# Kernel tuning notes

Measured on AMD Instinct MI355X. Metric: run time of the kernel, lower is better.

## Reference

```python
import jax, jax.numpy as jnp
import numpy as np

B, C, CI, H, W = 4, 256, 128, 48, 48
EPS = 1e-5  # BatchNorm2d default eps


def _make_bn(k, n, c):
    kg, kb, km, kv = jax.random.split(k, 4)
    gamma = 1.0 + 0.1 * jax.random.normal(kg, (n, c), jnp.float32)
    beta = 0.1 * jax.random.normal(kb, (n, c), jnp.float32)
    mean = 0.1 * jax.random.normal(km, (n, c), jnp.float32)
    var = 0.5 + jax.random.uniform(kv, (n, c), jnp.float32)
    return jnp.stack([gamma, beta, mean, var], axis=1)  # [n, 4, c]


def setup_inputs() -> dict:
    key = jax.random.key(0)
    ks = jax.random.split(key, 8)
    x1 = jax.random.normal(ks[0], (B, C, H, W), jnp.float32)
    x2 = jax.random.normal(ks[1], (B, C, H, W), jnp.float32)
    bn_pre = _make_bn(ks[2], 4, C)                       # g1, g2, theta, phi pre-BN
    w_pre = 0.05 * jax.random.normal(ks[3], (4, CI, C), jnp.float32)
    b_pre = 0.01 * jax.random.normal(ks[4], (4, CI), jnp.float32)
    w_post = 0.05 * jax.random.normal(ks[5], (2, C, CI), jnp.float32)  # W1, W2 convs
    b_post = 0.01 * jax.random.normal(ks[6], (2, C), jnp.float32)
    bn_post = _make_bn(ks[7], 2, C)                      # W1, W2 post-BN
    return dict(x1=x1, x2=x2, bn_pre=bn_pre, w_pre=w_pre, b_pre=b_pre,
                w_post=w_post, b_post=b_post, bn_post=bn_post)


def _bn(x, p):
    # eval-mode BatchNorm2d: p = [gamma, beta, mean, var], each [C]
    gamma, beta, mean, var = p[0], p[1], p[2], p[3]
    scale = (gamma / jnp.sqrt(var + EPS))[:, None, None]
    return (x - mean[:, None, None]) * scale + beta[:, None, None]


def reference(x1, x2, bn_pre, w_pre, b_pre, w_post, b_post, bn_post):
    Bsz, _, Hh, Ww = x1.shape
    N = Hh * Ww

    def pre(x, i):  # BN -> 1x1 conv -> flatten to [B, CI, N]
        h = _bn(x, bn_pre[i])
        y = jnp.einsum('oc,bchw->bohw', w_pre[i], h) + b_pre[i][None, :, None, None]
        return y.reshape(Bsz, -1, N)

    g11 = pre(x1, 0)   # g1(x1)
    g21 = pre(x2, 1)   # g2(x2)
    th1 = pre(x1, 2)   # theta(x1)
    ph1 = pre(x2, 3)   # phi(x2)

    e_time = jnp.einsum('bcn,bdn->bcd', th1, ph1)    # [B, CI, CI]  (theta @ phi^T)
    e_space = jnp.einsum('bcn,bcm->bnm', th1, ph1)   # [B, N, N]    (theta^T @ phi)

    et1s = jax.nn.softmax(e_time, axis=-1)                          # energy_time_1s
    et2s = jax.nn.softmax(jnp.swapaxes(e_time, 1, 2), axis=-1)      # energy_time_2s
    es2s = jax.nn.softmax(e_space, axis=-2)                         # energy_space_2s
    es1s = jax.nn.softmax(jnp.swapaxes(e_space, 1, 2), axis=-2)     # energy_space_1s

    y1 = jnp.einsum('bcd,bdn,bnm->bcm', et2s, g11, es2s).reshape(Bsz, -1, Hh, Ww)
    y2 = jnp.einsum('bcd,bdn,bnm->bcm', et1s, g21, es1s).reshape(Bsz, -1, Hh, Ww)

    def post(y, i):  # 1x1 conv -> BN
        h = jnp.einsum('oc,bchw->bohw', w_post[i], y) + b_post[i][None, :, None, None]
        return _bn(h, bn_post[i])

    return (x1 + post(y1, 0), x2 + post(y2, 1))
```

## Files before the change

### kernel.cpp

```cpp
#include <hip/hip_runtime.h>
#include <hip/hip_bf16.h>


#define N_PIX 2304
#define NB 4

typedef __attribute__((ext_vector_type(8))) short bf16x8;
typedef __attribute__((ext_vector_type(4))) float f32x4;

__device__ __forceinline__ short f2bf(float f) {
  unsigned u = __float_as_uint(f);
  unsigned r = (u + 0x7fffu + ((u >> 16) & 1u)) >> 16;
  return (short)r;
}
__device__ __forceinline__ float bf2f(short s) {
  return __uint_as_float(((unsigned)(unsigned short)s) << 16);
}
__device__ __forceinline__ int swzf(int row, int kc, int bk64) {
  return bk64 ? (kc ^ ((row ^ (row >> 3)) & 7)) : ((kc ^ (row >> 1)) & 3);
}
__device__ __forceinline__ unsigned pk2(short a, short b) {
  return (unsigned)(unsigned short)a | ((unsigned)(unsigned short)b << 16);
}


struct GArgs {
  const short *a0, *a1, *al0, *al1;
  const short *b0, *b1, *bl0, *bl1;
  long sa, sb, sal, sbl;
  int lda, ldb, lal, lbl;
  int K, ksplit, kchunk;
  int bt0, bt1;
  void *o0, *o1; long so;
  void *p0, *p1; long sp;
  void *q0, *q1; long sq;
  void *u0, *u1; long su;
  const float *aux0, *aux1; long saux;
  const float *res0, *res1; long sres;
};

template <int EPI, int SPLIT, int BK>
__global__ __launch_bounds__(256) void mgemm(GArgs g) {
  constexpr int NCHS = (BK == 64) ? 3 : 2;
  constexpr int ROWSH = (BK == 64) ? 6 : 5;
  constexpr int BK64 = (BK == 64);

  int z = blockIdx.z;
  int pb = z / g.ksplit, ks = z - pb * g.ksplit;
  int sel = pb >> 2, batch = pb & 3;
  const short* A = (sel ? g.a1 : g.a0) + (long)batch * g.sa;
  const short* B = (sel ? g.b1 : g.b0) + (long)batch * g.sb;
  const short* Al = nullptr; const short* Bl = nullptr;
  if (SPLIT) {
    Al = (sel ? g.al1 : g.al0) + (long)batch * g.sal;
    Bl = (sel ? g.bl1 : g.bl0) + (long)batch * g.sbl;
  }
  int bt = sel ? g.bt1 : g.bt0;
  int k0 = ks * g.kchunk, k1 = k0 + g.kchunk;
  int m0 = blockIdx.y << 7, n0 = blockIdx.x << 7;

  __shared__ short As[128 * BK];
  __shared__ short Bs[128 * BK];
  __shared__ short Als[SPLIT ? 128 * BK : 8];
  __shared__ short Bls[SPLIT ? 128 * BK : 8];

  int t = threadIdx.x;
  int lane = t & 63, wid = t >> 6;
  int wm = (wid >> 1) << 6, wn = (wid & 1) << 6;
  int l15 = lane & 15, lg = lane >> 4;

  f32x4 acc[4][4];
  #pragma unroll
  for (int i = 0; i < 4; ++i)
    #pragma unroll
    for (int j = 0; j < 4; ++j) acc[i][j] = (f32x4){0.f, 0.f, 0.f, 0.f};

  for (int kt = k0; kt < k1; kt += BK) {
    __syncthreads();
    #pragma unroll
    for (int i = 0; i < BK / 16; ++i) {
      int ch = t + (i << 8);
      int row = ch >> NCHS, kc = ch & ((BK >> 3) - 1);
      int di = (row << ROWSH) + (swzf(row, kc, BK64) << 3);
      *(bf16x8*)&As[di] = *(const bf16x8*)&A[(long)(m0 + row) * g.lda + kt + (kc << 3)];
      if (SPLIT)
        *(bf16x8*)&Als[di] = *(const bf16x8*)&Al[(long)(m0 + row) * g.lal + kt + (kc << 3)];
    }
    if (BK64 && bt) {
      int nc = t & 15, kq = t >> 4;
      const short* Bp = &B[(long)(kt + (kq << 2)) * g.ldb + n0 + (nc << 3)];
      bf16x8 v0 = *(const bf16x8*)&Bp[0];
      bf16x8 v1 = *(const bf16x8*)&Bp[g.ldb];
      bf16x8 v2 = *(const bf16x8*)&Bp[2 * g.ldb];
      bf16x8 v3 = *(const bf16x8*)&Bp[3 * g.ldb];
      int kc = kq >> 1, wof = (kq & 1) << 2;
      #pragma unroll
      for (int e = 0; e < 8; ++e) {
        int rn = (nc << 3) + e;
        uint2 pkk; pkk.x = pk2(v0[e], v1[e]); pkk.y = pk2(v2[e], v3[e]);
        *(uint2*)&Bs[(rn << 6) + (swzf(rn, kc, 1) << 3) + wof] = pkk;
      }
    } else {
      #pragma unroll
      for (int i = 0; i < BK / 16; ++i) {
        int ch = t + (i << 8);
        int row = ch >> NCHS, kc = ch & ((BK >> 3) - 1);
        int di = (row << ROWSH) + (swzf(row, kc, BK64) << 3);
        *(bf16x8*)&Bs[di] = *(const bf16x8*)&B[(long)(n0 + row) * g.ldb + kt + (kc << 3)];
        if (SPLIT)
          *(bf16x8*)&Bls[di] = *(const bf16x8*)&Bl[(long)(n0 + row) * g.lbl + kt + (kc << 3)];
      }
    }
    __syncthreads();
    #pragma unroll
    for (int ksub = 0; ksub < BK / 32; ++ksub) {
      int kb = (ksub << 2) + lg;
      bf16x8 ah[4], bh[4], alv[4], blv[4];
      #pragma unroll
      for (int i = 0; i < 4; ++i) {
        int ra = wm + (i << 4) + l15;
        int rb = wn + (i << 4) + l15;
        ah[i] = *(const bf16x8*)&As[(ra << ROWSH) + (swzf(ra, kb, BK64) << 3)];
        bh[i] = *(const bf16x8*)&Bs[(rb << ROWSH) + (swzf(rb, kb, BK64) << 3)];
        if (SPLIT) {
          alv[i] = *(const bf16x8*)&Als[(ra << ROWSH) + (swzf(ra, kb, BK64) << 3)];
          blv[i] = *(const bf16x8*)&Bls[(rb << ROWSH) + (swzf(rb, kb, BK64) << 3)];
        }
      }
      #pragma unroll
      for (int i = 0; i < 4; ++i)
        #pragma unroll
        for (int j = 0; j < 4; ++j) {
          if (SPLIT) {
            acc[i][j] = __builtin_amdgcn_mfma_f32_16x16x32_bf16(alv[i], bh[j], acc[i][j], 0, 0, 0);
            acc[i][j] = __builtin_amdgcn_mfma_f32_16x16x32_bf16(ah[i], blv[j], acc[i][j], 0, 0, 0);
          }
          acc[i][j] = __builtin_amdgcn_mfma_f32_16x16x32_bf16(ah[i], bh[j], acc[i][j], 0, 0, 0);
        }
    }
  }

  float rsacc[16];
  float cs4[4];
  if (EPI == 2) {
    #pragma unroll
    for (int q = 0; q < 16; ++q) rsacc[q] = 0.f;
  }
  #pragma unroll
  for (int j = 0; j < 4; ++j) {
    int col = n0 + wn + (j << 4) + l15;
    float csacc = 0.f;
    #pragma unroll
    for (int i = 0; i < 4; ++i) {
      int row0 = m0 + wm + (i << 4) + (lg << 2);
      if (EPI == 0) {
        const float* bias = (sel ? g.aux1 : g.aux0);
        short* FTB_ = (short*)(sel ? g.q1 : g.q0) + (long)batch * g.sq;
        float v[4]; short hh[4];
        #pragma unroll
        for (int r = 0; r < 4; ++r) { v[r] = acc[i][j][r] + bias[row0 + r]; hh[r] = f2bf(v[r]); }
        uint2 pk; pk.x = pk2(hh[0], hh[1]); pk.y = pk2(hh[2], hh[3]);
        *(uint2*)&FTB_[(long)col * 256 + row0] = pk;
        if (row0 >= 128) {
          short* FB_  = (short*)(sel ? g.o1 : g.o0) + (long)batch * g.so;
          short* FLO_ = (short*)(sel ? g.p1 : g.p0) + (long)batch * g.sp;
          short* FTL_ = (short*)(sel ? g.u1 : g.u0) + (long)batch * g.su;
          short ll[4];
          #pragma unroll
          for (int r = 0; r < 4; ++r) {
            ll[r] = f2bf(v[r] - bf2f(hh[r]));
            FB_[(long)(row0 - 128 + r) * N_PIX + col] = hh[r];
            FLO_[(long)(row0 - 128 + r) * N_PIX + col] = ll[r];
          }
          uint2 pl; pl.x = pk2(ll[0], ll[1]); pl.y = pk2(ll[2], ll[3]);
          *(uint2*)&FTL_[(long)col * 128 + (row0 - 128)] = pl;
        }
      } else if (EPI == 1) {
        float* ETP_ = (float*)g.o0 + ((long)ks * 4 + batch) * 16384;
        #pragma unroll
        for (int r = 0; r < 4; ++r) ETP_[(long)(row0 + r) * 128 + col] = acc[i][j][r];
      } else if (EPI == 2) {
        short* PT_ = (short*)g.o0 + (long)batch * g.so;
        short hh[4];
        #pragma unroll
        for (int r = 0; r < 4; ++r) {
          float ev = __expf(acc[i][j][r]);
          hh[r] = f2bf(ev);
          csacc += ev;
          rsacc[(i << 2) + r] += ev;
        }
        uint2 pk; pk.x = pk2(hh[0], hh[1]); pk.y = pk2(hh[2], hh[3]);
        *(uint2*)&PT_[(long)col * N_PIX + row0] = pk;
      } else if (EPI == 3) {
        short* AB_ = (short*)(sel ? g.o1 : g.o0) + (long)batch * g.so;
        #pragma unroll
        for (int r = 0; r < 4; ++r) AB_[(long)(row0 + r) * N_PIX + col] = f2bf(acc[i][j][r]);
      } else if (EPI == 6) {
        float* YTF_ = (float*)g.o0 + ((long)ks * 8 + sel * 4 + batch) * g.so;
        *(f32x4*)&YTF_[(long)col * 128 + row0] = acc[i][j];
      } else {
        float* O_ = (float*)(sel ? g.o1 : g.o0) + (long)batch * g.so;
        const float* bias = (sel ? g.aux1 : g.aux0);
        const float* R_ = (sel ? g.res1 : g.res0) + (long)batch * g.sres;
        #pragma unroll
        for (int r = 0; r < 4; ++r)
          O_[(long)(row0 + r) * N_PIX + col] =
              acc[i][j][r] + bias[row0 + r] + R_[(long)(row0 + r) * N_PIX + col];
      }
    }
    if (EPI == 2) {
      csacc += __shfl_xor(csacc, 16, 64);
      csacc += __shfl_xor(csacc, 32, 64);
      cs4[j] = csacc;
    }
  }
  if (EPI == 2) {
    #pragma unroll
    for (int i = 0; i < 4; ++i)
      #pragma unroll
      for (int r = 0; r < 4; ++r) {
        float v = rsacc[(i << 2) + r];
        v += __shfl_xor(v, 1, 64);
        v += __shfl_xor(v, 2, 64);
        v += __shfl_xor(v, 4, 64);
        v += __shfl_xor(v, 8, 64);
        rsacc[(i << 2) + r] = v;
      }
    __syncthreads();
    float* scr = (float*)&As[0];
    float* scr2 = (float*)&Bs[0];
    int rowhalf = wid >> 1, colhalf = wid & 1;
    if (lg == 0) {
      #pragma unroll
      for (int j = 0; j < 4; ++j) scr[rowhalf * 128 + wn + (j << 4) + l15] = cs4[j];
    }
    if (l15 == 0) {
      #pragma unroll
      for (int i = 0; i < 4; ++i)
        #pragma unroll
        for (int r = 0; r < 4; ++r)
          scr2[colhalf * 128 + wm + (i << 4) + (lg << 2) + r] = rsacc[(i << 2) + r];
    }
    __syncthreads();
    if (t < 128) {
      float* CSP_ = (float*)g.p0 + ((long)blockIdx.y * 4 + batch) * N_PIX;
      CSP_[n0 + t] = scr[t] + scr[128 + t];
    } else {
      int lr = t - 128;
      float* RSP_ = (float*)g.q0 + ((long)blockIdx.x * 4 + batch) * N_PIX;
      RSP_[m0 + lr] = scr2[lr] + scr2[128 + lr];
    }
  }
}


__global__ __launch_bounds__(256) void xcast(const float* __restrict__ x1,
                                             const float* __restrict__ x2,
                                             short* __restrict__ XH, short* __restrict__ XL) {
  __shared__ float tile[32][33];
  int z = blockIdx.z; int sel = z >> 2, b = z & 3;
  const float* X = (sel ? x2 : x1) + (long)b * 256 * N_PIX;
  long obase = ((long)(sel * 4 + b)) * N_PIX * 256;
  int n0 = blockIdx.x << 5, c0 = blockIdx.y << 5;
  int tx = threadIdx.x & 31, ty = threadIdx.x >> 5;
  #pragma unroll
  for (int i = 0; i < 4; ++i)
    tile[ty + (i << 3)][tx] = X[(long)(c0 + ty + (i << 3)) * N_PIX + n0 + tx];
  __syncthreads();
  #pragma unroll
  for (int i = 0; i < 4; ++i) {
    int n = n0 + ty + (i << 3);
    float v = tile[tx][ty + (i << 3)];
    short h = f2bf(v);
    XH[obase + (long)n * 256 + c0 + tx] = h;
    XL[obase + (long)n * 256 + c0 + tx] = f2bf(v - bf2f(h));
  }
}

__global__ __launch_bounds__(256) void fold_pre(const float* __restrict__ bn,
                                                const float* __restrict__ w,
                                                const float* __restrict__ b,
                                                short* __restrict__ WH, short* __restrict__ WL,
                                                float* __restrict__ Bc) {
  int blk = blockIdx.x;
  int xsel = blk >> 8, row = blk & 255;
  int i = (row < 128) ? xsel : (2 + xsel);
  int o = row & 127;
  int c = threadIdx.x;
  const float* bni = bn + i * 1024;
  float gm = bni[c], be = bni[256 + c], mn = bni[512 + c], vr = bni[768 + c];
  float s = gm * rsqrtf(vr + 1e-5f);
  float tb = be - mn * s;
  float wv = w[(i * 128 + o) * 256 + c];
  float val = wv * s;
  short h = f2bf(val);
  long idx = (long)(xsel * 256 + row) * 256 + c;
  WH[idx] = h;
  WL[idx] = f2bf(val - bf2f(h));
  __shared__ float red[256];
  red[c] = wv * tb;
  __syncthreads();
  for (int off = 128; off > 0; off >>= 1) {
    if (c < off) red[c] += red[c + off];
    __syncthreads();
  }
  if (c == 0) Bc[xsel * 256 + row] = b[i * 128 + o] + red[0];
}

__global__ __launch_bounds__(128) void fold_post(const float* __restrict__ bn,
                                                 const float* __restrict__ w,
                                                 const float* __restrict__ b,
                                                 short* __restrict__ WB, float* __restrict__ Bc) {
  int blk = blockIdx.x;
  int i = blk >> 8, o = blk & 255;
  const float* bni = bn + i * 1024;
  float s = bni[o] * rsqrtf(bni[768 + o] + 1e-5f);
  int c = threadIdx.x;
  long idx = (long)(i * 256 + o) * 128 + c;
  WB[idx] = f2bf(w[idx] * s);
  if (c == 0) Bc[i * 256 + o] = b[i * 256 + o] * s + bni[256 + o] - bni[512 + o] * s;
}

__global__ __launch_bounds__(256) void ereduce(const float* __restrict__ ETP,
                                               float* __restrict__ ET) {
  int idx = blockIdx.x * 256 + threadIdx.x;
  int b = idx >> 14, e = idx & 16383;
  float s = 0.f;
  #pragma unroll
  for (int ks = 0; ks < 36; ++ks) s += ETP[((long)ks * 4 + b) * 16384 + e];
  ET[(long)b * 16384 + e] = s;
}

__global__ __launch_bounds__(256) void et_softmax(const float* __restrict__ Et,
                                                  short* __restrict__ MB) {
  __shared__ float Es[128 * 129];
  int b = blockIdx.x, t = threadIdx.x;
  const float* E = Et + (long)b * 16384;
  for (int i = t; i < 16384; i += 256) {
    int r = i >> 7, c = i & 127;
    Es[r * 129 + c] = E[i];
  }
  __syncthreads();
  short* M1 = MB + (long)b * 16384;
  short* M2 = MB + (long)(4 + b) * 16384;
  if (t < 128) {
    float rm = -1e30f;
    for (int j = 0; j < 128; ++j) rm = fmaxf(rm, Es[t * 129 + j]);
    float rs = 0.f;
    for (int j = 0; j < 128; ++j) rs += __expf(Es[t * 129 + j] - rm);
    float ri = 1.0f / rs;
    for (int j = 0; j < 128; ++j) M2[t * 128 + j] = f2bf(__expf(Es[t * 129 + j] - rm) * ri);
  } else {
    int c = t - 128;
    float cm = -1e30f;
    for (int d = 0; d < 128; ++d) cm = fmaxf(cm, Es[d * 129 + c]);
    float cs = 0.f;
    for (int d = 0; d < 128; ++d) cs += __expf(Es[d * 129 + c] - cm);
    float ci = 1.0f / cs;
    for (int d = 0; d < 128; ++d) M1[c * 128 + d] = f2bf(__expf(Es[d * 129 + c] - cm) * ci);
  }
}

__global__ __launch_bounds__(256) void csrs_reduce(const float* __restrict__ CSP,
                                                   const float* __restrict__ RSP,
                                                   float* __restrict__ CS,
                                                   float* __restrict__ RS) {
  int idx = blockIdx.x * 256 + threadIdx.x;
  int which = idx / 9216;
  int rem = idx - which * 9216;
  int b = rem / N_PIX, col = rem - b * N_PIX;
  const float* P = which ? RSP : CSP;
  float s = 0.f;
  #pragma unroll
  for (int k = 0; k < 18; ++k) s += P[((long)k * 4 + b) * N_PIX + col];
  (which ? RS : CS)[b * N_PIX + col] = s;
}

__global__ __launch_bounds__(256) void yreduce(const float* __restrict__ YTF,
                                               const float* __restrict__ CS,
                                               const float* __restrict__ RS,
                                               short* __restrict__ YT) {
  const long PSTR = 8L * 2304 * 128;
  long idx = ((long)blockIdx.x * 256 + threadIdx.x) << 3;
  long z = idx / 294912;
  long rem = idx - z * 294912;
  int col = (int)(rem >> 7);
  int sel = (int)(z >> 2), b = (int)(z & 3);
  const float* S = sel ? RS : CS;
  float inv = 1.0f / S[b * N_PIX + col];
  float4 a0 = *(const float4*)&YTF[idx];
  float4 a1 = *(const float4*)&YTF[idx + 4];
  float4 b0 = *(const float4*)&YTF[PSTR + idx];
  float4 b1 = *(const float4*)&YTF[PSTR + idx + 4];
  float4 c0 = *(const float4*)&YTF[2 * PSTR + idx];
  float4 c1 = *(const float4*)&YTF[2 * PSTR + idx + 4];
  bf16x8 o;
  o[0] = f2bf((a0.x + b0.x + c0.x) * inv); o[1] = f2bf((a0.y + b0.y + c0.y) * inv);
  o[2] = f2bf((a0.z + b0.z + c0.z) * inv); o[3] = f2bf((a0.w + b0.w + c0.w) * inv);
  o[4] = f2bf((a1.x + b1.x + c1.x) * inv); o[5] = f2bf((a1.y + b1.y + c1.y) * inv);
  o[6] = f2bf((a1.z + b1.z + c1.z) * inv); o[7] = f2bf((a1.w + b1.w + c1.w) * inv);
  *(bf16x8*)&YT[idx] = o;
}

extern "C" void kernel_launch(void* const* d_in, const int* in_sizes, int n_in,
                              void* d_out, int out_size, void* d_ws, size_t ws_size,
                              hipStream_t stream) {
  const float* x1 = (const float*)d_in[0];
  const float* x2 = (const float*)d_in[1];
  const float* bn_pre = (const float*)d_in[2];
  const float* w_pre = (const float*)d_in[3];
  const float* b_pre = (const float*)d_in[4];
  const float* w_post = (const float*)d_in[5];
  const float* b_post = (const float*)d_in[6];
  const float* bn_post = (const float*)d_in[7];
  float* out = (float*)d_out;

  char* W = (char*)d_ws;
  float* CS    = (float*)(W + 0);
  float* RS    = (float*)(W + 36864);
  float* BPRE  = (float*)(W + 73728);
  float* BPOST = (float*)(W + 75776);
  float* ET    = (float*)(W + 77824);
  short* WPREH = (short*)(W + 339968);
  short* WPREL = (short*)(W + 602112);
  short* WPOSTB= (short*)(W + 864256);
  short* MB    = (short*)(W + 995328);
  short* XTH   = (short*)(W + 1257472);
  short* XTL   = (short*)(W + 10694656);
  short* FB    = (short*)(W + 20131840);
  short* FLO   = (short*)(W + 24850432);
  short* FTB   = (short*)(W + 29569024);
  short* FTLO  = (short*)(W + 39006208);
  short* AB    = (short*)(W + 43724800);
  short* YT    = (short*)(W + 48443392);
  short* PT    = (short*)(W + 53161984);
  float* YTF   = (float*)(W + 95629312);
  float* CSP   = (float*)(W + 95629312);
  float* RSP   = (float*)(W + 95629312 + 663552);

  xcast<<<dim3(72, 8, 8), 256, 0, stream>>>(x1, x2, XTH, XTL);
  fold_pre<<<512, 256, 0, stream>>>(bn_pre, w_pre, b_pre, WPREH, WPREL, BPRE);
  fold_post<<<512, 128, 0, stream>>>(bn_post, w_post, b_post, WPOSTB, BPOST);

  { GArgs g{};
    g.a0 = WPREH; g.a1 = WPREH + 65536; g.al0 = WPREL; g.al1 = WPREL + 65536;
    g.sa = 0; g.sal = 0; g.lda = 256; g.lal = 256;
    g.b0 = XTH; g.b1 = XTH + 4L * 2304 * 256; g.bl0 = XTL; g.bl1 = XTL + 4L * 2304 * 256;
    g.sb = 2304L * 256; g.sbl = 2304L * 256; g.ldb = 256; g.lbl = 256;
    g.K = 256; g.ksplit = 1; g.kchunk = 256; g.bt0 = 0; g.bt1 = 0;
    g.o0 = FB; g.o1 = FB + 4L * 128 * 2304; g.so = 128L * 2304;
    g.p0 = FLO; g.p1 = FLO + 4L * 128 * 2304; g.sp = 128L * 2304;
    g.q0 = FTB; g.q1 = FTB + 4L * 2304 * 256; g.sq = 2304L * 256;
    g.u0 = FTLO; g.u1 = FTLO + 4L * 2304 * 128; g.su = 2304L * 128;
    g.aux0 = BPRE; g.aux1 = BPRE + 256; g.saux = 0;
    mgemm<0, 1, 32><<<dim3(18, 2, 8), 256, 0, stream>>>(g); }

  { GArgs g{};
    g.a0 = g.a1 = FB; g.al0 = g.al1 = FLO;
    g.sa = g.sal = 128L * 2304; g.lda = g.lal = 2304;
    g.b0 = g.b1 = FB + 4L * 128 * 2304; g.bl0 = g.bl1 = FLO + 4L * 128 * 2304;
    g.sb = g.sbl = 128L * 2304; g.ldb = g.lbl = 2304;
    g.K = 2304; g.ksplit = 36; g.kchunk = 64; g.bt0 = 0; g.bt1 = 0;
    g.o0 = g.o1 = YTF; g.so = 16384;
    mgemm<1, 1, 32><<<dim3(1, 1, 144), 256, 0, stream>>>(g); }

  ereduce<<<256, 256, 0, stream>>>(YTF, ET);
  et_softmax<<<4, 256, 0, stream>>>(ET, MB);

  { GArgs g{};
    g.a0 = g.a1 = FTB + 128; g.al0 = g.al1 = FTLO;
    g.sa = 2304L * 256; g.sal = 2304L * 128; g.lda = 256; g.lal = 128;
    g.b0 = g.b1 = FTB + 4L * 2304 * 256 + 128; g.bl0 = g.bl1 = FTLO + 4L * 2304 * 128;
    g.sb = 2304L * 256; g.sbl = 2304L * 128; g.ldb = 256; g.lbl = 128;
    g.K = 128; g.ksplit = 1; g.kchunk = 128; g.bt0 = 0; g.bt1 = 0;
    g.o0 = g.o1 = PT; g.so = (long)2304 * 2304;
    g.p0 = CSP; g.q0 = RSP;
    mgemm<2, 1, 32><<<dim3(18, 18, 4), 256, 0, stream>>>(g); }

  csrs_reduce<<<72, 256, 0, stream>>>(CSP, RSP, CS, RS);

  { GArgs g{};
    g.a0 = MB; g.a1 = MB + 4 * 16384; g.sa = 16384; g.lda = 128;
    g.b0 = FTB; g.b1 = FTB + 4L * 2304 * 256; g.sb = 2304L * 256; g.ldb = 256;
    g.K = 128; g.ksplit = 1; g.kchunk = 128; g.bt0 = 0; g.bt1 = 0;
    g.o0 = AB; g.o1 = AB + 4L * 128 * 2304; g.so = 128L * 2304;
    mgemm<3, 0, 64><<<dim3(18, 1, 8), 256, 0, stream>>>(g); }

  { GArgs g{};
    g.a0 = AB; g.a1 = AB + 4L * 128 * 2304; g.sa = 128L * 2304; g.lda = 2304;
    g.b0 = g.b1 = PT; g.sb = (long)2304 * 2304; g.ldb = 2304;
    g.K = 2304; g.ksplit = 3; g.kchunk = 768; g.bt0 = 0; g.bt1 = 1;
    g.o0 = g.o1 = YTF; g.so = 2304L * 128;
    mgemm<6, 0, 64><<<dim3(18, 1, 24), 256, 0, stream>>>(g); }

  yreduce<<<1152, 256, 0, stream>>>(YTF, CS, RS, YT);

  { GArgs g{};
    g.a0 = WPOSTB; g.a1 = WPOSTB + 32768; g.sa = 0; g.lda = 128;
    g.b0 = YT; g.b1 = YT + 4L * 2304 * 128; g.sb = 2304L * 128; g.ldb = 128;
    g.K = 128; g.ksplit = 1; g.kchunk = 128; g.bt0 = 0; g.bt1 = 0;
    g.o0 = out; g.o1 = out + 4L * 256 * 2304; g.so = 256L * 2304;
    g.aux0 = BPOST; g.aux1 = BPOST + 256; g.saux = 0;
    g.res0 = x1; g.res1 = x2; g.sres = 256L * 2304;
    mgemm<5, 0, 64><<<dim3(18, 2, 8), 256, 0, stream>>>(g); }
}
```

Before: 238.4 us.

## Use direct global-to-LDS loads and stage exp tile through LDS for coalesced stores

Replaces the register round-trip for A/B tile loads with global_load_lds, moving the swizzle onto the global source address so data lands directly in shared memory. It also restructures the EPI==2 epilogue so the exponentiated tile is first written transposed into swizzled LDS and then written to global memory as coalesced 16-byte rows, instead of scattered 8-byte transposed stores. This aims to cut VGPR pressure and load latency in the main loop and to improve write coalescing of the large N×N probability matrix. The LDS-direct path depends on wave-uniform LDS base addressing being correct for the swizzled layout.

Result: no change. 235.3 us (-1.3%).

```diff
diff --git a/kernel.cpp b/kernel.cpp
--- a/kernel.cpp
+++ b/kernel.cpp
@@ -21,6 +21,10 @@
 }
 __device__ __forceinline__ unsigned pk2(short a, short b) {
   return (unsigned)(unsigned short)a | ((unsigned)(unsigned short)b << 16);
+}
+__device__ __forceinline__ void gll16(const short* g, short* l) {
+  __builtin_amdgcn_global_load_lds((const __attribute__((address_space(1))) void*)g,
+                                   (__attribute__((address_space(3))) void*)l, 16, 0, 0);
 }
 
 
@@ -44,6 +48,7 @@
   constexpr int NCHS = (BK == 64) ? 3 : 2;
   constexpr int ROWSH = (BK == 64) ? 6 : 5;
   constexpr int BK64 = (BK == 64);
+  constexpr int NT = SPLIT ? 4 : 2;
 
   int z = blockIdx.z;
   int pb = z / g.ksplit, ks = z - pb * g.ksplit;
@@ -59,10 +64,11 @@
   int k0 = ks * g.kchunk, k1 = k0 + g.kchunk;
   int m0 = blockIdx.y << 7, n0 = blockIdx.x << 7;
 
-  __shared__ short As[128 * BK];
-  __shared__ short Bs[128 * BK];
-  __shared__ short Als[SPLIT ? 128 * BK : 8];
-  __shared__ short Bls[SPLIT ? 128 * BK : 8];
+  __shared__ short SM[NT * 128 * BK];
+  short* As = SM;
+  short* Bs = SM + 128 * BK;
+  short* Als = SM + (SPLIT ? 2 : 0) * 128 * BK;
+  short* Bls = SM + (SPLIT ? 3 : 0) * 128 * BK;
 
   int t = threadIdx.x;
   int lane = t & 63, wid = t >> 6;
@@ -81,10 +87,11 @@
     for (int i = 0; i < BK / 16; ++i) {
       int ch = t + (i << 8);
       int row = ch >> NCHS, kc = ch & ((BK >> 3) - 1);
-      int di = (row << ROWSH) + (swzf(row, kc, BK64) << 3);
-      *(bf16x8*)&As[di] = *(const bf16x8*)&A[(long)(m0 + row) * g.lda + kt + (kc << 3)];
+      int kcs = swzf(row, kc, BK64);
+      int lb = (i << 11) + (wid << 9);
+      gll16(&A[(long)(m0 + row) * g.lda + kt + (kcs << 3)], As + lb);
       if (SPLIT)
-        *(bf16x8*)&Als[di] = *(const bf16x8*)&Al[(long)(m0 + row) * g.lal + kt + (kc << 3)];
+        gll16(&Al[(long)(m0 + row) * g.lal + kt + (kcs << 3)], Als + lb);
     }
     if (BK64 && bt) {
       int nc = t & 15, kq = t >> 4;
@@ -105,10 +112,11 @@
       for (int i = 0; i < BK / 16; ++i) {
         int ch = t + (i << 8);
         int row = ch >> NCHS, kc = ch & ((BK >> 3) - 1);
-        int di = (row << ROWSH) + (swzf(row, kc, BK64) << 3);
-        *(bf16x8*)&Bs[di] = *(const bf16x8*)&B[(long)(n0 + row) * g.ldb + kt + (kc << 3)];
+        int kcs = swzf(row, kc, BK64);
+        int lb = (i << 11) + (wid << 9);
+        gll16(&B[(long)(n0 + row) * g.ldb + kt + (kcs << 3)], Bs + lb);
         if (SPLIT)
-          *(bf16x8*)&Bls[di] = *(const bf16x8*)&Bl[(long)(n0 + row) * g.lbl + kt + (kc << 3)];
+          gll16(&Bl[(long)(n0 + row) * g.lbl + kt + (kcs << 3)], Bls + lb);
       }
     }
     __syncthreads();
@@ -140,16 +148,83 @@
     }
   }
 
-  float rsacc[16];
-  float cs4[4];
   if (EPI == 2) {
+    float rsacc[16];
     #pragma unroll
     for (int q = 0; q < 16; ++q) rsacc[q] = 0.f;
-  }
+    float cs4[4];
+    __syncthreads();
+    #pragma unroll
+    for (int j = 0; j < 4; ++j) {
+      int c = wn + (j << 4) + l15;
+      float csacc = 0.f;
+      #pragma unroll
+      for (int i = 0; i < 4; ++i) {
+        short hh[4];
+        #pragma unroll
+        for (int r = 0; r < 4; ++r) {
+          float ev = __expf(acc[i][j][r]);
+          hh[r] = f2bf(ev);
+          csacc += ev;
+          rsacc[(i << 2) + r] += ev;
+        }
+        uint2 pk; pk.x = pk2(hh[0], hh[1]); pk.y = pk2(hh[2], hh[3]);
+        int u8 = (wm >> 2) + (i << 2) + lg;
+        ((uint2*)SM)[(c << 5) + (u8 ^ ((c & 15) << 1))] = pk;
+      }
+      csacc += __shfl_xor(csacc, 16, 64);
+      csacc += __shfl_xor(csacc, 32, 64);
+      cs4[j] = csacc;
+    }
+    #pragma unroll
+    for (int i = 0; i < 4; ++i)
+      #pragma unroll
+      for (int r = 0; r < 4; ++r) {
+        float v = rsacc[(i << 2) + r];
+        v += __shfl_xor(v, 1, 64);
+        v += __shfl_xor(v, 2, 64);
+        v += __shfl_xor(v, 4, 64);
+        v += __shfl_xor(v, 8, 64);
+        rsacc[(i << 2) + r] = v;
+      }
+    __syncthreads();
+    short* PT_ = (short*)g.o0 + (long)batch * g.so;
+    #pragma unroll
+    for (int p = 0; p < 8; ++p) {
+      int cc = (p << 4) + (t >> 4);
+      bf16x8 v = *(bf16x8*)&SM[(cc << 7) + (((t & 15) ^ (cc & 15)) << 3)];
+      *(bf16x8*)&PT_[(long)(n0 + cc) * N_PIX + m0 + ((t & 15) << 3)] = v;
+    }
+    __syncthreads();
+    float* scr = (float*)SM;
+    float* scr2 = scr + 256;
+    int rowhalf = wid >> 1, colhalf = wid & 1;
+    if (lg == 0) {
+      #pragma unroll
+      for (int j = 0; j < 4; ++j) scr[rowhalf * 128 + wn + (j << 4) + l15] = cs4[j];
+    }
+    if (l15 == 0) {
+      #pragma unroll
+      for (int i = 0; i < 4; ++i)
+        #pragma unroll
+        for (int r = 0; r < 4; ++r)
+          scr2[colhalf * 128 + wm + (i << 4) + (lg << 2) + r] = rsacc[(i << 2) + r];
+    }
+    __syncthreads();
+    if (t < 128) {
+      float* CSP_ = (float*)g.p0 + ((long)blockIdx.y * 4 + batch) * N_PIX;
+      CSP_[n0 + t] = scr[t] + scr[128 + t];
+    } else {
+      int lr = t - 128;
+      float* RSP_ = (float*)g.q0 + ((long)blockIdx.x * 4 + batch) * N_PIX;
+      RSP_[m0 + lr] = scr2[lr] + scr2[128 + lr];
+    }
+    return;
+  }
+
   #pragma unroll
   for (int j = 0; j < 4; ++j) {
     int col = n0 + wn + (j << 4) + l15;
-    float csacc = 0.f;
     #pragma unroll
     for (int i = 0; i < 4; ++i) {
       int row0 = m0 + wm + (i << 4) + (lg << 2);
@@ -179,18 +254,6 @@
         float* ETP_ = (float*)g.o0 + ((long)ks * 4 + batch) * 16384;
         #pragma unroll
         for (int r = 0; r < 4; ++r) ETP_[(long)(row0 + r) * 128 + col] = acc[i][j][r];
-      } else if (EPI == 2) {
-        short* PT_ = (short*)g.o0 + (long)batch * g.so;
-        short hh[4];
-        #pragma unroll
-        for (int r = 0; r < 4; ++r) {
-          float ev = __expf(acc[i][j][r]);
-          hh[r] = f2bf(ev);
-          csacc += ev;
-          rsacc[(i << 2) + r] += ev;
-        }
-        uint2 pk; pk.x = pk2(hh[0], hh[1]); pk.y = pk2(hh[2], hh[3]);
-        *(uint2*)&PT_[(long)col * N_PIX + row0] = pk;
       } else if (EPI == 3) {
         short* AB_ = (short*)(sel ? g.o1 : g.o0) + (long)batch * g.so;
         #pragma unroll
@@ -207,48 +270,6 @@
           O_[(long)(row0 + r) * N_PIX + col] =
               acc[i][j][r] + bias[row0 + r] + R_[(long)(row0 + r) * N_PIX + col];
       }
-    }
-    if (EPI == 2) {
-      csacc += __shfl_xor(csacc, 16, 64);
-      csacc += __shfl_xor(csacc, 32, 64);
-      cs4[j] = csacc;
-    }
-  }
-  if (EPI == 2) {
-    #pragma unroll
-    for (int i = 0; i < 4; ++i)
-      #pragma unroll
-      for (int r = 0; r < 4; ++r) {
-        float v = rsacc[(i << 2) + r];
-        v += __shfl_xor(v, 1, 64);
-        v += __shfl_xor(v, 2, 64);
-        v += __shfl_xor(v, 4, 64);
-        v += __shfl_xor(v, 8, 64);
-        rsacc[(i << 2) + r] = v;
-      }
-    __syncthreads();
-    float* scr = (float*)&As[0];
-    float* scr2 = (float*)&Bs[0];
-    int rowhalf = wid >> 1, colhalf = wid & 1;
-    if (lg == 0) {
-      #pragma unroll
-      for (int j = 0; j < 4; ++j) scr[rowhalf * 128 + wn + (j << 4) + l15] = cs4[j];
-    }
-    if (l15 == 0) {
-      #pragma unroll
-      for (int i = 0; i < 4; ++i)
-        #pragma unroll
-        for (int r = 0; r < 4; ++r)
-          scr2[colhalf * 128 + wm + (i << 4) + (lg << 2) + r] = rsacc[(i << 2) + r];
-    }
-    __syncthreads();
-    if (t < 128) {
-      float* CSP_ = (float*)g.p0 + ((long)blockIdx.y * 4 + batch) * N_PIX;
-      CSP_[n0 + t] = scr[t] + scr[128 + t];
-    } else {
-      int lr = t - 128;
-      float* RSP_ = (float*)g.q0 + ((long)blockIdx.x * 4 + batch) * N_PIX;
-      RSP_[m0 + lr] = scr2[lr] + scr2[128 + lr];
     }
   }
 }
```
